# Optimization experiments

Measured on AMD Instinct MI355X. Metric: run time of the kernel, lower is better.

## Reference

```python
import jax, jax.numpy as jnp
import numpy as np

NEG_SLOPE = 0.01  # torch F.leaky_relu default

def _leaky(v):
    return jnp.where(v > 0, v, NEG_SLOPE * v)

def _gcn_conv(h, W, b, row, col, n_nodes):
    # PyG GCNConv with add_self_loops=True, symmetric normalization:
    # out = D^{-1/2} (A + I) D^{-1/2} (h @ W) + b,  deg includes self loop (+1)
    xw = h @ W                                            # [N, H]
    deg = jnp.zeros((n_nodes,), xw.dtype).at[col].add(1.0) + 1.0
    dis = jax.lax.rsqrt(deg)
    norm = dis[row] * dis[col]                            # [E]
    agg = jnp.zeros_like(xw).at[col].add(norm[:, None] * xw[row])
    agg = agg + xw * (1.0 / deg)[:, None]                 # self-loop term: dis_i^2 = 1/deg_i
    return agg + b

def setup_inputs() -> dict:
    key = jax.random.key(0)
    ks = jax.random.split(key, 16)
    N, E, EL = 100000, 1600000, 200000
    IN, H, EA = 256, 64, 8
    s = 0.05
    return {
        "x": jax.random.normal(ks[0], (N, IN), jnp.float32),
        "edge_index": jax.random.randint(ks[1], (2, E), 0, N, jnp.int64),
        "edge_label_index": jax.random.randint(ks[2], (2, EL), 0, N, jnp.int64),
        "edge_attr": jax.random.normal(ks[3], (EL, EA), jnp.float32),
        "W1": jax.random.normal(ks[4], (IN, 128), jnp.float32) * s,
        "b1": jnp.zeros((128,), jnp.float32),
        "W2": jax.random.normal(ks[5], (128, H), jnp.float32) * s,
        "b2": jnp.zeros((H,), jnp.float32),
        "Wg1": jax.random.normal(ks[6], (H, H), jnp.float32) * s,
        "bg1": jnp.zeros((H,), jnp.float32),
        "Wg2": jax.random.normal(ks[7], (H, H), jnp.float32) * s,
        "bg2": jnp.zeros((H,), jnp.float32),
        "Wp": jax.random.normal(ks[8], (2 * H + EA, 1), jnp.float32) * s,
        "bp": jnp.zeros((1,), jnp.float32),
    }

def reference(x, edge_index, edge_label_index, edge_attr,
              W1, b1, W2, b2, Wg1, bg1, Wg2, bg2, Wp, bp):
    n_nodes = x.shape[0]
    row, col = edge_index[0], edge_index[1]
    # preprocess MLP (dropout p=0.0 -> identity)
    h = _leaky(x @ W1 + b1)
    h = _leaky(h @ W2 + b2)
    # two GCN layers
    h = _leaky(_gcn_conv(h, Wg1, bg1, row, col, n_nodes))
    h = _leaky(_gcn_conv(h, Wg2, bg2, row, col, n_nodes))
    # edge scoring head: gather-concat-linear
    h_src = h[edge_label_index[0]]
    h_dst = h[edge_label_index[1]]
    combined = jnp.concatenate([h_src, h_dst, edge_attr], axis=1)
    out = (combined @ Wp + bp).reshape(-1)
    return (out, h)
```

## Files before the change

### kernel.cpp

```cpp
#include <hip/hip_runtime.h>
#include <hip/hip_bf16.h>

typedef __attribute__((ext_vector_type(8))) short bf16x8;
typedef __attribute__((ext_vector_type(4))) float f32x4;

#define BSHIFT 8
#define BW 256
#define NSTR 8
#define BCAP 768
#define LCAP 24
#define KEDGE 16

__device__ __forceinline__ float lk(float v) { return v > 0.f ? v : 0.01f * v; }

__device__ __forceinline__ short f2b(float v) {
  union { __hip_bfloat16 h; short s; } u;
  u.h = __float2bfloat16(v);
  return u.s;
}
__device__ __forceinline__ float loadF(const void* p, size_t i, int f32) {
  return f32 ? ((const float*)p)[i]
             : __bfloat162float(((const __hip_bfloat16*)p)[i]);
}
__device__ __forceinline__ void storeF(void* p, size_t i, int f32, float v) {
  if (f32) ((float*)p)[i] = v;
  else     ((__hip_bfloat16*)p)[i] = __float2bfloat16(v);
}
__device__ __forceinline__ int loadI(const int* p, size_t base, size_t e, int i64) {
  return i64 ? p[2 * (base + e)] : p[base + e];
}
__device__ __forceinline__ float blo(unsigned u) {
  union { unsigned u; float f; } c; c.u = u << 16; return c.f;
}
__device__ __forceinline__ float bhi(unsigned u) {
  union { unsigned u; float f; } c; c.u = u & 0xffff0000u; return c.f;
}

__global__ void detect_kernel(const unsigned short* __restrict__ x,
                              const int* __restrict__ ei, int* __restrict__ flags) {
  int t = threadIdx.x;
  unsigned short u = x[t];
  int ex = (u >> 7) & 0xFF;
  if (ex >= 0xC0) atomicOr(&flags[0], 1);
  if (t < 128 && ei[2 * t + 1] != 0) atomicOr(&flags[1], 1);
}

__global__ __launch_bounds__(64) void pack_w_kernel(const void* __restrict__ W,
                                                    __hip_bfloat16* __restrict__ P,
                                                    int N, const int* __restrict__ flags) {
  int f32 = flags[0] != 0;
  int ks = blockIdx.x, ct = blockIdx.y, KS = gridDim.x;
  int lane = threadIdx.x;
  int g = lane >> 4, m = lane & 15;
  size_t base = ((size_t)(ct * KS + ks) * 64 + (size_t)lane) * 8;
#pragma unroll
  for (int j = 0; j < 8; ++j)
    P[base + j] = __float2bfloat16(
        loadF(W, (size_t)(ks * 32 + g * 8 + j) * N + (size_t)(ct * 16 + m), f32));
}


template <int ROWB, int F32>
__device__ __forceinline__ void stage_tile(const char* __restrict__ Ab, char* tile,
                                           int row0, int M, int w, int lane) {
  constexpr int CPR = ROWB / 16;
  constexpr int PERW = 32 * CPR / 4;
#pragma unroll
  for (int i = 0; i < PERW; i += 64) {
    int p = w * PERW + i + lane;
    int r = p / CPR;
    int pc = p - r * CPR;
    int xv = F32 ? ((r & 3) << 1) : (r & 7);
    int gr = row0 + r; if (gr >= M) gr = M - 1;
    const char* src = Ab + (size_t)gr * ROWB + (size_t)(pc ^ xv) * 16;
    char* dst = tile + (size_t)(w * PERW + i) * 16;
    __builtin_amdgcn_global_load_lds(
        (const __attribute__((address_space(1))) void*)src,
        (__attribute__((address_space(3))) void*)dst, 16, 0, 0);
  }
}

template <int KS, int CT, int F32>
__device__ __forceinline__ void tile_core(const char* tile,
                                          const __hip_bfloat16* __restrict__ bbase,
                                          int m, int g, f32x4 (&accs)[2][CT]) {
  constexpr int ROWB = KS * 32 * (F32 ? 4 : 2);
#pragma unroll
  for (int ks = 0; ks < KS; ++ks) {
    bf16x8 a[2];
#pragma unroll
    for (int t = 0; t < 2; ++t) {
      int r = t * 16 + m;
      if constexpr (F32) {
        int c = ks * 8 + g * 2;
        int xv = (r & 3) << 1;
        float4 q0 = *(const float4*)(tile + (size_t)r * ROWB + (size_t)((c ^ xv) * 16));
        float4 q1 = *(const float4*)(tile + (size_t)r * ROWB + (size_t)(((c + 1) ^ xv) * 16));
        a[t][0] = f2b(q0.x); a[t][1] = f2b(q0.y); a[t][2] = f2b(q0.z); a[t][3] = f2b(q0.w);
        a[t][4] = f2b(q1.x); a[t][5] = f2b(q1.y); a[t][6] = f2b(q1.z); a[t][7] = f2b(q1.w);
      } else {
        int c = ks * 4 + g;
        int xv = r & 7;
        a[t] = *(const bf16x8*)(tile + (size_t)r * ROWB + (size_t)((c ^ xv) * 16));
      }
    }
    const __hip_bfloat16* bb = bbase + (size_t)ks * 64 * 8;
#pragma unroll
    for (int cc = 0; cc < CT; ++cc) {
      bf16x8 b = *(const bf16x8*)(bb + (size_t)cc * KS * 64 * 8);
#pragma unroll
      for (int t = 0; t < 2; ++t)
        accs[t][cc] = __builtin_amdgcn_mfma_f32_16x16x32_bf16(a[t], b, accs[t][cc], 0, 0, 0);
    }
  }
}

template <int KS, int CT, int AMODE>
__global__ __launch_bounds__(256) void gemm_tiled(const void* __restrict__ A,
                                                  const __hip_bfloat16* __restrict__ Bp,
                                                  const void* __restrict__ bias,
                                                  void* __restrict__ Out, int out_bf16,
                                                  __hip_bfloat16* __restrict__ Yout,
                                                  const float* __restrict__ dinv,
                                                  int M, int N, int act,
                                                  const int* __restrict__ flags) {
  constexpr int K = KS * 32;
  constexpr int LDSB = 32 * K * (AMODE ? 4 : 2);
  __shared__ char tile[LDSB];
  int f32 = AMODE ? (flags[0] != 0) : 0;
  int lane = threadIdx.x & 63;
  int w = threadIdx.x >> 6;
  int m = lane & 15, g = lane >> 4;
  int row0 = blockIdx.x * 32;

  const char* Ab = (const char*)A;
  if (f32) stage_tile<K * 4, 1>(Ab, tile, row0, M, w, lane);
  else     stage_tile<K * 2, 0>(Ab, tile, row0, M, w, lane);
  __syncthreads();

  const __hip_bfloat16* bbase = Bp + ((size_t)(w * CT) * KS * 64 + (size_t)lane) * 8;
  f32x4 accs[2][CT];
#pragma unroll
  for (int t = 0; t < 2; ++t)
#pragma unroll
    for (int cc = 0; cc < CT; ++cc) accs[t][cc] = (f32x4){0, 0, 0, 0};

  if (f32) tile_core<KS, CT, 1>(tile, bbase, m, g, accs);
  else     tile_core<KS, CT, 0>(tile, bbase, m, g, accs);

  float bv[CT];
#pragma unroll
  for (int cc = 0; cc < CT; ++cc)
    bv[cc] = bias ? loadF(bias, (size_t)((w * CT + cc) * 16 + m), flags[0] != 0) : 0.f;
#pragma unroll
  for (int t = 0; t < 2; ++t) {
#pragma unroll
    for (int r = 0; r < 4; ++r) {
      int ro = row0 + t * 16 + g * 4 + r;
      if (ro < M) {
        float di = Yout ? dinv[ro] : 0.f;
#pragma unroll
        for (int cc = 0; cc < CT; ++cc) {
          int col = (w * CT + cc) * 16 + m;
          float v = accs[t][cc][r] + bv[cc];
          if (act) v = lk(v);
          if (Out) {
            if (out_bf16) ((__hip_bfloat16*)Out)[(size_t)ro * N + col] = __float2bfloat16(v);
            else          ((float*)Out)[(size_t)ro * N + col] = v;
          }
          if (Yout) Yout[(size_t)ro * N + col] = __float2bfloat16(v * di);
        }
      }
    }
  }
}

__global__ __launch_bounds__(256) void bin_kernel(const int* __restrict__ ei,
                                                  int* __restrict__ cur,
                                                  int2* __restrict__ rec,
                                                  int E, int NB,
                                                  const int* __restrict__ flags) {
  extern __shared__ int lds[];
  int* bcnt = lds;
  int* gbase = lds + NB;
  int2* bins = (int2*)(lds + 2 * NB);
  int i64 = flags[1] == 0;
  int stripe = __builtin_amdgcn_s_getreg(63508) & (NSTR - 1);
  int t = threadIdx.x;
  const int perRound = 256 * KEDGE;
  for (int base = blockIdx.x * perRound; base < E; base += gridDim.x * perRound) {
    for (int b = t; b < NB; b += 256) bcnt[b] = 0;
    __syncthreads();
#pragma unroll 1
    for (int k = 0; k < KEDGE; ++k) {
      int i = base + k * 256 + t;
      if (i < E) {
        int r = loadI(ei, 0, (size_t)i, i64);
        int c = loadI(ei, (size_t)E, (size_t)i, i64);
        int b = c >> BSHIFT;
        int pos = atomicAdd(&bcnt[b], 1);
        if (pos < LCAP) {
          bins[b * LCAP + pos] = make_int2(r, c);
        } else {
          int bs = b * NSTR + stripe;
          int slot = atomicAdd(&cur[bs], 1);
          if (slot < BCAP) rec[(size_t)bs * BCAP + slot] = make_int2(r, c);
        }
      }
    }
    __syncthreads();
    for (int b = t; b < NB; b += 256) {
      int n = min(bcnt[b], LCAP);
      if (n > 0) gbase[b] = atomicAdd(&cur[b * NSTR + stripe], n);
    }
    __syncthreads();
    int lane = t & 63, w = t >> 6;
    for (int b = w; b < NB; b += 4) {
      int n = min(bcnt[b], LCAP);
      if (n == 0) continue;
      int gb = gbase[b];
      size_t sb = (size_t)(b * NSTR + stripe) * BCAP;
      if (lane < n && gb + lane < BCAP)
        rec[sb + gb + lane] = bins[b * LCAP + lane];
    }
    __syncthreads();
  }
}

__global__ __launch_bounds__(512) void bucket_scan(const int* __restrict__ cur,
                                                   int* __restrict__ bbase, int NB) {
  __shared__ int lds[512];
  int t = threadIdx.x;
  int tot = 0;
  if (t < NB)
#pragma unroll
    for (int s = 0; s < NSTR; ++s) tot += min(cur[t * NSTR + s], BCAP);
  lds[t] = tot; __syncthreads();
  for (int o = 1; o < 512; o <<= 1) {
    int a = (t >= o) ? lds[t - o] : 0; __syncthreads();
    lds[t] += a; __syncthreads();
  }
  if (t < NB) bbase[t] = lds[t] - tot;
}

__global__ __launch_bounds__(256) void place_kernel(const int2* __restrict__ rec,
                                                    const int* __restrict__ cur,
                                                    const int* __restrict__ bbase,
                                                    int* __restrict__ rowptr,
                                                    int* __restrict__ csr,
                                                    float* __restrict__ dinv, int Nn) {
  int b = blockIdx.x;
  int lo = b << BSHIFT;
  int t = threadIdx.x;
  __shared__ int cnt[BW];
  __shared__ int sc[BW];
  __shared__ int cursor[BW];
  cnt[t] = 0;
  __syncthreads();
#pragma unroll 1
  for (int s = 0; s < NSTR; ++s) {
    int n = min(cur[b * NSTR + s], BCAP);
    const int2* rp = rec + (size_t)(b * NSTR + s) * BCAP;
    for (int j = t; j < n; j += 256) atomicAdd(&cnt[rp[j].y - lo], 1);
  }
  __syncthreads();
  int v = cnt[t];
  sc[t] = v; __syncthreads();
  for (int o = 1; o < BW; o <<= 1) {
    int a = (t >= o) ? sc[t - o] : 0; __syncthreads();
    sc[t] += a; __syncthreads();
  }
  int base = bbase[b];
  int col = lo + t;
  if (col < Nn) {
    rowptr[col] = base + sc[t];
    dinv[col] = rsqrtf((float)v + 1.0f);
  }
  cursor[t] = base + sc[t] - v;
  __syncthreads();
#pragma unroll 1
  for (int s = 0; s < NSTR; ++s) {
    int n = min(cur[b * NSTR + s], BCAP);
    const int2* rp = rec + (size_t)(b * NSTR + s) * BCAP;
    for (int j = t; j < n; j += 256) {
      int2 e = rp[j];
      int pos = atomicAdd(&cursor[e.y - lo], 1);
      csr[pos] = e.x;
    }
  }
}

__global__ __launch_bounds__(256) void gather_kernel(const __hip_bfloat16* __restrict__ y,
                                                     const int* __restrict__ csr,
                                                     const int* __restrict__ rowptr,
                                                     const float* __restrict__ dinv,
                                                     const void* __restrict__ bias,
                                                     void* __restrict__ outp, size_t obase,
                                                     int out_use_flag, int Nn,
                                                     float* __restrict__ ssrc,
                                                     float* __restrict__ sdst,
                                                     const void* __restrict__ Wp,
                                                     const int* __restrict__ flags) {
  int f32 = flags[0] != 0;
  int of32 = out_use_flag ? f32 : 0;
  int lane = threadIdx.x & 63;
  int node = (blockIdx.x * blockDim.x + threadIdx.x) >> 6;
  if (node >= Nn) return;
  int s = (node == 0) ? 0 : rowptr[node - 1];
  int e = rowptr[node];
  int half = lane >> 5;
  int hl = lane & 31;
  int f = hl * 2;
  const unsigned* yu = (const unsigned*)y;
  float p0a = 0, p1a = 0, p0b = 0, p1b = 0;
  float p0c = 0, p1c = 0, p0d = 0, p1d = 0;
  for (int base = s; base < e; base += 64) {
    int cnt = e - base; if (cnt > 64) cnt = 64;
    int rl = (base + lane < e) ? csr[base + lane] : 0;
    int j = 0;
    for (; j + 8 <= cnt; j += 8) {
      int r0 = __shfl(rl, j + half, 64);
      int r1 = __shfl(rl, j + 2 + half, 64);
      int r2 = __shfl(rl, j + 4 + half, 64);
      int r3 = __shfl(rl, j + 6 + half, 64);
      unsigned u0 = yu[(unsigned)r0 * 32u + hl];
      unsigned u1 = yu[(unsigned)r1 * 32u + hl];
      unsigned u2 = yu[(unsigned)r2 * 32u + hl];
      unsigned u3 = yu[(unsigned)r3 * 32u + hl];
      p0a += blo(u0); p1a += bhi(u0);
      p0b += blo(u1); p1b += bhi(u1);
      p0c += blo(u2); p1c += bhi(u2);
      p0d += blo(u3); p1d += bhi(u3);
    }
    for (; j + 2 <= cnt; j += 2) {
      int r0 = __shfl(rl, j + half, 64);
      unsigned u0 = yu[(unsigned)r0 * 32u + hl];
      p0a += blo(u0); p1a += bhi(u0);
    }
    if (j < cnt) {
      int r0 = __shfl(rl, j, 64);
      if (half == 0) {
        unsigned u0 = yu[(unsigned)r0 * 32u + hl];
        p0a += blo(u0); p1a += bhi(u0);
      }
    }
  }
  float acc0 = (p0a + p0b) + (p0c + p0d);
  float acc1 = (p1a + p1b) + (p1c + p1d);
  acc0 += __shfl_xor(acc0, 32, 64);
  acc1 += __shfl_xor(acc1, 32, 64);
  unsigned un = yu[(unsigned)node * 32u + hl];
  acc0 += blo(un); acc1 += bhi(un);
  float di = dinv[node];
  float v0 = lk(di * acc0 + loadF(bias, (size_t)f, f32));
  float v1 = lk(di * acc1 + loadF(bias, (size_t)(f + 1), f32));
  if (half == 0) {
    if (of32) {
      *(float2*)((float*)outp + obase + (size_t)node * 64 + f) = make_float2(v0, v1);
    } else {
      union { unsigned u; unsigned short s[2]; } pk;
      pk.s[0] = (unsigned short)f2b(v0);
      pk.s[1] = (unsigned short)f2b(v1);
      *(unsigned*)((__hip_bfloat16*)outp + obase + (size_t)node * 64 + f) = pk.u;
    }
  }
  if (ssrc) {
    float q1 = v0 * loadF(Wp, (size_t)f, f32) + v1 * loadF(Wp, (size_t)(f + 1), f32);
    float q2 = v0 * loadF(Wp, (size_t)(64 + f), f32) + v1 * loadF(Wp, (size_t)(65 + f), f32);
#pragma unroll
    for (int o = 16; o > 0; o >>= 1) {
      q1 += __shfl_down(q1, o, 64);
      q2 += __shfl_down(q2, o, 64);
    }
    if (lane == 0) { ssrc[node] = q1; sdst[node] = q2; }
  }
}

__global__ __launch_bounds__(256) void edge_head_kernel(void* __restrict__ dout,
                                                        const int* __restrict__ eli,
                                                        const void* __restrict__ ea,
                                                        const float* __restrict__ ssrc,
                                                        const float* __restrict__ sdst,
                                                        const void* __restrict__ Wp,
                                                        const void* __restrict__ bp,
                                                        int EL, const int* __restrict__ flags) {
  int f32 = flags[0] != 0;
  int i64 = flags[1] == 0;
  int tid = blockIdx.x * blockDim.x + threadIdx.x;
  if (tid >= EL) return;
  int s = loadI(eli, 0, (size_t)tid, i64);
  int d = loadI(eli, (size_t)EL, (size_t)tid, i64);
  float acc = ssrc[s] + sdst[d] + loadF(bp, 0, f32);
  if (f32) {
    const float* eap = (const float*)ea + (size_t)tid * 8;
    float4 u0 = *(const float4*)eap;
    float4 u1 = *(const float4*)(eap + 4);
    acc += u0.x * loadF(Wp, 128, 1) + u0.y * loadF(Wp, 129, 1) +
           u0.z * loadF(Wp, 130, 1) + u0.w * loadF(Wp, 131, 1) +
           u1.x * loadF(Wp, 132, 1) + u1.y * loadF(Wp, 133, 1) +
           u1.z * loadF(Wp, 134, 1) + u1.w * loadF(Wp, 135, 1);
  } else {
    bf16x8 u = *(const bf16x8*)((const __hip_bfloat16*)ea + (size_t)tid * 8);
#pragma unroll
    for (int j = 0; j < 8; ++j) {
      union { short s; __hip_bfloat16 h; } cv; cv.s = u[j];
      acc += __bfloat162float(cv.h) * loadF(Wp, (size_t)(128 + j), 0);
    }
  }
  storeF(dout, (size_t)tid, f32, acc);
}

extern "C" void kernel_launch(void* const* d_in, const int* in_sizes, int n_in,
                              void* d_out, int out_size, void* d_ws, size_t ws_size,
                              hipStream_t stream) {
  const void* x   = d_in[0];
  const int* ei   = (const int*)d_in[1];
  const int* eli  = (const int*)d_in[2];
  const void* ea  = d_in[3];
  const void* W1  = d_in[4];
  const void* b1  = d_in[5];
  const void* W2  = d_in[6];
  const void* b2  = d_in[7];
  const void* Wg1 = d_in[8];
  const void* bg1 = d_in[9];
  const void* Wg2 = d_in[10];
  const void* bg2 = d_in[11];
  const void* Wp  = d_in[12];
  const void* bp  = d_in[13];

  const int Nn = in_sizes[0] / 256;
  const int E  = in_sizes[1] / 2;
  const int EL = in_sizes[2] / 2;
  const int NB = (Nn + BW - 1) >> BSHIFT;

  char* ws = (char*)d_ws;
  size_t off = 0;
  auto take = [&](size_t bytes) -> char* {
    char* p = ws + off;
    off = (off + bytes + 255) & ~(size_t)255;
    return p;
  };
  int*   flags  = (int*)take(256);
  int*   cur    = (int*)take((size_t)NB * NSTR * 4);
  int*   bbase  = (int*)take((size_t)NB * 4);
  int*   rowptr = (int*)take((size_t)Nn * 4);
  float* dinv   = (float*)take((size_t)Nn * 4);
  float* ssrc   = (float*)take((size_t)Nn * 4);
  float* sdst   = (float*)take((size_t)Nn * 4);
  int*   csr    = (int*)take((size_t)E * 4);
  int2*  rec    = (int2*)take((size_t)NB * NSTR * BCAP * 8);
  __hip_bfloat16* pW1 = (__hip_bfloat16*)take(256 * 128 * 2);
  __hip_bfloat16* pW2 = (__hip_bfloat16*)take(128 * 64 * 2);
  __hip_bfloat16* pG1 = (__hip_bfloat16*)take(64 * 64 * 2);
  __hip_bfloat16* pG2 = (__hip_bfloat16*)take(64 * 64 * 2);
  char* regionA = take((size_t)Nn * 128 * 4);
  char* regionB = take((size_t)Nn * 64 * 4);
  __hip_bfloat16* h1 = (__hip_bfloat16*)regionA;
  __hip_bfloat16* y = (__hip_bfloat16*)(regionA + (size_t)Nn * 64 * 4);
  __hip_bfloat16* h2 = (__hip_bfloat16*)regionB;
  __hip_bfloat16* h3 = (__hip_bfloat16*)regionB;

  hipMemsetAsync(flags, 0, 256 + (((size_t)NB * NSTR * 4 + 255) & ~(size_t)255), stream);
  detect_kernel<<<1, 256, 0, stream>>>((const unsigned short*)x, ei, flags);

  dim3 b64(64);
  pack_w_kernel<<<dim3(8, 8), b64, 0, stream>>>(W1, pW1, 128, flags);
  pack_w_kernel<<<dim3(4, 4), b64, 0, stream>>>(W2, pW2, 64, flags);
  pack_w_kernel<<<dim3(2, 4), b64, 0, stream>>>(Wg1, pG1, 64, flags);
  pack_w_kernel<<<dim3(2, 4), b64, 0, stream>>>(Wg2, pG2, 64, flags);

  const int ldsbytes = NB * (8 + LCAP * 8);
  const int nbin = (E + 256 * KEDGE - 1) / (256 * KEDGE);
  bin_kernel<<<nbin, 256, ldsbytes, stream>>>(ei, cur, rec, E, NB, flags);
  bucket_scan<<<1, 512, 0, stream>>>(cur, bbase, NB);
  place_kernel<<<NB, 256, 0, stream>>>(rec, cur, bbase, rowptr, csr, dinv, Nn);

  const int tblocks = (Nn + 31) / 32;
  gemm_tiled<8, 2, 1><<<tblocks, 256, 0, stream>>>(x, pW1, b1, h1, 1, nullptr, nullptr,
                                                   Nn, 128, 1, flags);
  gemm_tiled<4, 1, 0><<<tblocks, 256, 0, stream>>>(h1, pW2, b2, h2, 1, nullptr, nullptr,
                                                   Nn, 64, 1, flags);

  gemm_tiled<2, 1, 0><<<tblocks, 256, 0, stream>>>(h2, pG1, nullptr, nullptr, 0, y, dinv,
                                                   Nn, 64, 0, flags);
  gather_kernel<<<(Nn + 3) / 4, 256, 0, stream>>>(y, csr, rowptr, dinv, bg1,
                                                  h3, 0, 0, Nn,
                                                  nullptr, nullptr, nullptr, flags);

  gemm_tiled<2, 1, 0><<<tblocks, 256, 0, stream>>>(h3, pG2, nullptr, nullptr, 0, y, dinv,
                                                   Nn, 64, 0, flags);
  gather_kernel<<<(Nn + 3) / 4, 256, 0, stream>>>(y, csr, rowptr, dinv, bg2,
                                                  d_out, (size_t)EL, 1, Nn,
                                                  ssrc, sdst, Wp, flags);

  edge_head_kernel<<<(EL + 255) / 256, 256, 0, stream>>>(d_out, eli, ea, ssrc, sdst,
                                                         Wp, bp, EL, flags);
}
```

Measured before the change: 417.5 us.

## Process two nodes per wave in GCN gather, widen place kernel, simplify edge loads

```diff
diff --git a/kernel.cpp b/kernel.cpp
--- a/kernel.cpp
+++ b/kernel.cpp
@@ -195,8 +195,14 @@
     for (int k = 0; k < KEDGE; ++k) {
       int i = base + k * 256 + t;
       if (i < E) {
-        int r = loadI(ei, 0, (size_t)i, i64);
-        int c = loadI(ei, (size_t)E, (size_t)i, i64);
+        int r, c;
+        if (i64) {
+          r = ((const int2*)ei)[i].x;
+          c = ((const int2*)ei)[(size_t)E + i].x;
+        } else {
+          r = ei[i];
+          c = ei[(size_t)E + i];
+        }
         int b = c >> BSHIFT;
         int pos = atomicAdd(&bcnt[b], 1);
         if (pos < LCAP) {
@@ -243,7 +249,7 @@
   if (t < NB) bbase[t] = lds[t] - tot;
 }
 
-__global__ __launch_bounds__(256) void place_kernel(const int2* __restrict__ rec,
+__global__ __launch_bounds__(512) void place_kernel(const int2* __restrict__ rec,
                                                     const int* __restrict__ cur,
                                                     const int* __restrict__ bbase,
                                                     int* __restrict__ rowptr,
@@ -255,34 +261,39 @@
   __shared__ int cnt[BW];
   __shared__ int sc[BW];
   __shared__ int cursor[BW];
-  cnt[t] = 0;
+  if (t < BW) cnt[t] = 0;
   __syncthreads();
 #pragma unroll 1
   for (int s = 0; s < NSTR; ++s) {
     int n = min(cur[b * NSTR + s], BCAP);
     const int2* rp = rec + (size_t)(b * NSTR + s) * BCAP;
-    for (int j = t; j < n; j += 256) atomicAdd(&cnt[rp[j].y - lo], 1);
+    for (int j = t; j < n; j += 512) atomicAdd(&cnt[rp[j].y - lo], 1);
   }
   __syncthreads();
-  int v = cnt[t];
-  sc[t] = v; __syncthreads();
+  int v = 0;
+  if (t < BW) { v = cnt[t]; sc[t] = v; }
+  __syncthreads();
   for (int o = 1; o < BW; o <<= 1) {
-    int a = (t >= o) ? sc[t - o] : 0; __syncthreads();
-    sc[t] += a; __syncthreads();
-  }
-  int base = bbase[b];
-  int col = lo + t;
-  if (col < Nn) {
-    rowptr[col] = base + sc[t];
-    dinv[col] = rsqrtf((float)v + 1.0f);
-  }
-  cursor[t] = base + sc[t] - v;
+    int a = (t >= o && t < BW) ? sc[t - o] : 0;
+    __syncthreads();
+    if (t < BW) sc[t] += a;
+    __syncthreads();
+  }
+  if (t < BW) {
+    int base = bbase[b];
+    int col = lo + t;
+    if (col < Nn) {
+      rowptr[col] = base + sc[t];
+      dinv[col] = rsqrtf((float)v + 1.0f);
+    }
+    cursor[t] = base + sc[t] - v;
+  }
   __syncthreads();
 #pragma unroll 1
   for (int s = 0; s < NSTR; ++s) {
     int n = min(cur[b * NSTR + s], BCAP);
     const int2* rp = rec + (size_t)(b * NSTR + s) * BCAP;
-    for (int j = t; j < n; j += 256) {
+    for (int j = t; j < n; j += 512) {
       int2 e = rp[j];
       int pos = atomicAdd(&cursor[e.y - lo], 1);
       csr[pos] = e.x;
@@ -304,25 +315,55 @@
   int f32 = flags[0] != 0;
   int of32 = out_use_flag ? f32 : 0;
   int lane = threadIdx.x & 63;
-  int node = (blockIdx.x * blockDim.x + threadIdx.x) >> 6;
-  if (node >= Nn) return;
-  int s = (node == 0) ? 0 : rowptr[node - 1];
-  int e = rowptr[node];
+  int w = (blockIdx.x * blockDim.x + threadIdx.x) >> 6;
+  if (2 * w >= Nn) return;
   int half = lane >> 5;
   int hl = lane & 31;
-  int f = hl * 2;
+  int hb = half << 5;
+  int node = 2 * w + half;
+  int alive = node < Nn;
+  int nd = alive ? node : Nn - 1;
+  int s = (nd == 0) ? 0 : rowptr[nd - 1];
+  int e = rowptr[nd];
+  if (!alive) e = s;
   const unsigned* yu = (const unsigned*)y;
   float p0a = 0, p1a = 0, p0b = 0, p1b = 0;
   float p0c = 0, p1c = 0, p0d = 0, p1d = 0;
-  for (int base = s; base < e; base += 64) {
-    int cnt = e - base; if (cnt > 64) cnt = 64;
-    int rl = (base + lane < e) ? csr[base + lane] : 0;
+  for (int base = s; base < e; base += 32) {
+    int cnt = e - base; if (cnt > 32) cnt = 32;
+    int rl = (base + hl < e) ? csr[base + hl] : 0;
     int j = 0;
     for (; j + 8 <= cnt; j += 8) {
-      int r0 = __shfl(rl, j + half, 64);
-      int r1 = __shfl(rl, j + 2 + half, 64);
-      int r2 = __shfl(rl, j + 4 + half, 64);
-      int r3 = __shfl(rl, j + 6 + half, 64);
+      int r0 = __shfl(rl, hb + j + 0, 64);
+      int r1 = __shfl(rl, hb + j + 1, 64);
+      int r2 = __shfl(rl, hb + j + 2, 64);
+      int r3 = __shfl(rl, hb + j + 3, 64);
+      int r4 = __shfl(rl, hb + j + 4, 64);
+      int r5 = __shfl(rl, hb + j + 5, 64);
+      int r6 = __shfl(rl, hb + j + 6, 64);
+      int r7 = __shfl(rl, hb + j + 7, 64);
+      unsigned u0 = yu[(unsigned)r0 * 32u + hl];
+      unsigned u1 = yu[(unsigned)r1 * 32u + hl];
+      unsigned u2 = yu[(unsigned)r2 * 32u + hl];
+      unsigned u3 = yu[(unsigned)r3 * 32u + hl];
+      unsigned u4 = yu[(unsigned)r4 * 32u + hl];
+      unsigned u5 = yu[(unsigned)r5 * 32u + hl];
+      unsigned u6 = yu[(unsigned)r6 * 32u + hl];
+      unsigned u7 = yu[(unsigned)r7 * 32u + hl];
+      p0a += blo(u0); p1a += bhi(u0);
+      p0b += blo(u1); p1b += bhi(u1);
+      p0c += blo(u2); p1c += bhi(u2);
+      p0d += blo(u3); p1d += bhi(u3);
+      p0a += blo(u4); p1a += bhi(u4);
+      p0b += blo(u5); p1b += bhi(u5);
+      p0c += blo(u6); p1c += bhi(u6);
+      p0d += blo(u7); p1d += bhi(u7);
+    }
+    for (; j + 4 <= cnt; j += 4) {
+      int r0 = __shfl(rl, hb + j + 0, 64);
+      int r1 = __shfl(rl, hb + j + 1, 64);
+      int r2 = __shfl(rl, hb + j + 2, 64);
+      int r3 = __shfl(rl, hb + j + 3, 64);
       unsigned u0 = yu[(unsigned)r0 * 32u + hl];
       unsigned u1 = yu[(unsigned)r1 * 32u + hl];
       unsigned u2 = yu[(unsigned)r2 * 32u + hl];
@@ -332,35 +373,27 @@
       p0c += blo(u2); p1c += bhi(u2);
       p0d += blo(u3); p1d += bhi(u3);
     }
-    for (; j + 2 <= cnt; j += 2) {
-      int r0 = __shfl(rl, j + half, 64);
+    for (; j < cnt; ++j) {
+      int r0 = __shfl(rl, hb + j, 64);
       unsigned u0 = yu[(unsigned)r0 * 32u + hl];
       p0a += blo(u0); p1a += bhi(u0);
     }
-    if (j < cnt) {
-      int r0 = __shfl(rl, j, 64);
-      if (half == 0) {
-        unsigned u0 = yu[(unsigned)r0 * 32u + hl];
-        p0a += blo(u0); p1a += bhi(u0);
-      }
-    }
   }
   float acc0 = (p0a + p0b) + (p0c + p0d);
   float acc1 = (p1a + p1b) + (p1c + p1d);
-  acc0 += __shfl_xor(acc0, 32, 64);
-  acc1 += __shfl_xor(acc1, 32, 64);
-  unsigned un = yu[(unsigned)node * 32u + hl];
+  unsigned un = yu[(unsigned)nd * 32u + hl];
   acc0 += blo(un); acc1 += bhi(un);
-  float di = dinv[node];
+  float di = dinv[nd];
+  int f = hl * 2;
   float v0 = lk(di * acc0 + loadF(bias, (size_t)f, f32));
   float v1 = lk(di * acc1 + loadF(bias, (size_t)(f + 1), f32));
-  if (half == 0) {
+  if (alive) {
     if (of32) {
       *(float2*)((float*)outp + obase + (size_t)node * 64 + f) = make_float2(v0, v1);
     } else {
-      union { unsigned u; unsigned short s[2]; } pk;
-      pk.s[0] = (unsigned short)f2b(v0);
-      pk.s[1] = (unsigned short)f2b(v1);
+      union { unsigned u; unsigned short ss[2]; } pk;
+      pk.ss[0] = (unsigned short)f2b(v0);
+      pk.ss[1] = (unsigned short)f2b(v1);
       *(unsigned*)((__hip_bfloat16*)outp + obase + (size_t)node * 64 + f) = pk.u;
     }
   }
@@ -372,7 +405,7 @@
       q1 += __shfl_down(q1, o, 64);
       q2 += __shfl_down(q2, o, 64);
     }
-    if (lane == 0) { ssrc[node] = q1; sdst[node] = q2; }
+    if (hl == 0 && alive) { ssrc[node] = q1; sdst[node] = q2; }
   }
 }
 
@@ -473,7 +506,7 @@
   const int nbin = (E + 256 * KEDGE - 1) / (256 * KEDGE);
   bin_kernel<<<nbin, 256, ldsbytes, stream>>>(ei, cur, rec, E, NB, flags);
   bucket_scan<<<1, 512, 0, stream>>>(cur, bbase, NB);
-  place_kernel<<<NB, 256, 0, stream>>>(rec, cur, bbase, rowptr, csr, dinv, Nn);
+  place_kernel<<<NB, 512, 0, stream>>>(rec, cur, bbase, rowptr, csr, dinv, Nn);
 
   const int tblocks = (Nn + 31) / 32;
   gemm_tiled<8, 2, 1><<<tblocks, 256, 0, stream>>>(x, pW1, b1, h1, 1, nullptr, nullptr,
@@ -481,17 +514,19 @@
   gemm_tiled<4, 1, 0><<<tblocks, 256, 0, stream>>>(h1, pW2, b2, h2, 1, nullptr, nullptr,
                                                    Nn, 64, 1, flags);
 
+  const int gwaves = (Nn + 1) / 2;
+  const int gblocks = (gwaves + 3) / 4;
   gemm_tiled<2, 1, 0><<<tblocks, 256, 0, stream>>>(h2, pG1, nullptr, nullptr, 0, y, dinv,
                                                    Nn, 64, 0, flags);
-  gather_kernel<<<(Nn + 3) / 4, 256, 0, stream>>>(y, csr, rowptr, dinv, bg1,
-                                                  h3, 0, 0, Nn,
-                                                  nullptr, nullptr, nullptr, flags);
+  gather_kernel<<<gblocks, 256, 0, stream>>>(y, csr, rowptr, dinv, bg1,
+                                             h3, 0, 0, Nn,
+                                             nullptr, nullptr, nullptr, flags);
 
   gemm_tiled<2, 1, 0><<<tblocks, 256, 0, stream>>>(h3, pG2, nullptr, nullptr, 0, y, dinv,
                                                    Nn, 64, 0, flags);
-  gather_kernel<<<(Nn + 3) / 4, 256, 0, stream>>>(y, csr, rowptr, dinv, bg2,
-                                                  d_out, (size_t)EL, 1, Nn,
-                                                  ssrc, sdst, Wp, flags);
+  gather_kernel<<<gblocks, 256, 0, stream>>>(y, csr, rowptr, dinv, bg2,
+                                             d_out, (size_t)EL, 1, Nn,
+                                             ssrc, sdst, Wp, flags);
 
   edge_head_kernel<<<(EL + 255) / 256, 256, 0, stream>>>(d_out, eli, ea, ssrc, sdst,
                                                          Wp, bp, EL, flags);
```

Measured after the change: 392.1 us. 1.06x faster.
